# Kernel tuning notes

Measured on AMD Instinct MI355X. Metric: run time of the kernel, lower is better.

The kernel has to match this reference:

```python
import jax, jax.numpy as jnp
import numpy as np

B, C, K, L = 2, 64, 256, 128
H = 8
DH = C // H
PROJ = 64
DADP = 10
FFT = 8
NG = 4
EPS = 1e-5
SCALE = float(1.0 / np.sqrt(DH))


def group_norm(x, g, b):
    # x: (B, C, N); GroupNorm(4, C)
    bb, cc, nn = x.shape
    xg = x.reshape(bb, NG, cc // NG, nn)
    mu = jnp.mean(xg, axis=(2, 3), keepdims=True)
    var = jnp.var(xg, axis=(2, 3), keepdims=True)
    xn = ((xg - mu) * jax.lax.rsqrt(var + EPS)).reshape(bb, cc, nn)
    return xn * g[None, :, None] + b[None, :, None]


def layer_norm(x, g, b):
    mu = jnp.mean(x, axis=-1, keepdims=True)
    var = jnp.var(x, axis=-1, keepdims=True)
    return (x - mu) * jax.lax.rsqrt(var + EPS) * g + b


def setup_inputs() -> dict:
    key = jax.random.key(0)
    ks = jax.random.split(key, 24)
    it = iter(ks)

    def nrm(shape, scale=0.05):
        return jax.random.normal(next(it), shape, dtype=jnp.float32) * scale

    z = lambda *s: jnp.zeros(s, jnp.float32)
    o = lambda *s: jnp.ones(s, jnp.float32)
    inp = dict(
        y=jax.random.normal(next(it), (B, C, K * L), dtype=jnp.float32),
        a1=jax.nn.softmax(jax.random.normal(next(it), (K, K), dtype=jnp.float32), axis=1),
        a2=jax.nn.softmax(jax.random.normal(next(it), (K, K), dtype=jnp.float32), axis=1),
        nodevec1=nrm((K, DADP), 0.3), nodevec2=nrm((DADP, K), 0.3),
        gcn_w=nrm((C, 7 * C)), gcn_b=z(C),
        s_wq=nrm((C, C)), s_wk=nrm((C, C)), s_wv=nrm((C, C)),
        s_pk=nrm((K, PROJ), float(1.0 / np.sqrt(PROJ))),
        s_pv=nrm((K, PROJ), float(1.0 / np.sqrt(PROJ))),
        s_wo=nrm((C, C)), s_bo=z(C),
        t_wq=nrm((C, C)), t_wk=nrm((C, C)), t_wv=nrm((C, C)),
        t_bq=z(C), t_bk=z(C), t_bv=z(C),
        t_wo=nrm((C, C)), t_bo=z(C),
        t_l1w=nrm((C, FFT)), t_l1b=z(FFT), t_l2w=nrm((FFT, C)), t_l2b=z(C),
        t_ln1g=o(C), t_ln1b=z(C), t_ln2g=o(C), t_ln2b=z(C),
        gn_local_g=o(C), gn_local_b=z(C),
        gn_s_g=o(C), gn_s_b=z(C),
        gn_t_g=o(C), gn_t_b=z(C),
        ff1_w=nrm((C, 2 * C)), ff1_b=z(2 * C),
        ff2_w=nrm((2 * C, C)), ff2_b=z(C),
        gn2_g=o(C), gn2_b=z(C),
        base_B=B, base_K=K, base_L=L,
    )
    return inp


def reference(y, a1, a2, nodevec1, nodevec2, gcn_w, gcn_b,
              s_wq, s_wk, s_wv, s_pk, s_pv, s_wo, s_bo,
              t_wq, t_wk, t_wv, t_bq, t_bk, t_bv, t_wo, t_bo,
              t_l1w, t_l1b, t_l2w, t_l2b, t_ln1g, t_ln1b, t_ln2g, t_ln2b,
              gn_local_g, gn_local_b, gn_s_g, gn_s_b, gn_t_g, gn_t_b,
              ff1_w, ff1_b, ff2_w, ff2_b, gn2_g, gn2_b,
              base_B, base_K, base_L):
    Bv, Kv, Lv = int(base_B), int(base_K), int(base_L)
    y4 = y.reshape(Bv, C, Kv, Lv)

    # ---- AdaptiveGCN: order-2 conv over [a1, a2, adaptive adj] + self ----
    x = y4.transpose(0, 3, 1, 2)  # (B, L, C, K)
    adp = jax.nn.softmax(jax.nn.relu(nodevec1 @ nodevec2), axis=1)  # (K, K)
    outs = [x]
    for a in (a1, a2, adp):
        x1 = jnp.einsum('blcv,wv->blcw', x, a)
        x2 = jnp.einsum('blcv,wv->blcw', x1, a)
        outs += [x1, x2]
    cat = jnp.concatenate(outs, axis=2)  # (B, L, 7C, K)
    g = jnp.einsum('blik,oi->blok', cat, gcn_w) + gcn_b[None, None, :, None]
    y_local = g.transpose(0, 2, 3, 1).reshape(Bv, C, Kv * Lv)
    y_local = group_norm(y + y_local, gn_local_g, gn_local_b)

    # ---- Linformer-style spatial attention over K ----
    xs = y4.transpose(0, 3, 2, 1).reshape(Bv * Lv, Kv, C)  # (B*L, K, C)
    q = (xs @ s_wq).reshape(-1, Kv, H, DH).transpose(0, 2, 1, 3)
    kp = jnp.einsum('bnd,nk->bkd', xs @ s_wk, s_pk).reshape(-1, PROJ, H, DH).transpose(0, 2, 1, 3)
    vp = jnp.einsum('bnd,nk->bkd', xs @ s_wv, s_pv).reshape(-1, PROJ, H, DH).transpose(0, 2, 1, 3)
    attn = jax.nn.softmax(jnp.einsum('bhnd,bhkd->bhnk', q, kp) * SCALE, axis=-1)
    o = jnp.einsum('bhnk,bhkd->bhnd', attn, vp).transpose(0, 2, 1, 3).reshape(-1, Kv, C)
    o = o @ s_wo + s_bo
    y_s = o.transpose(0, 2, 1).reshape(Bv, Lv, C, Kv).transpose(0, 2, 3, 1).reshape(Bv, C, Kv * Lv)
    y_s = group_norm(y + y_s, gn_s_g, gn_s_b)

    # ---- temporal transformer encoder layer over L ----
    xt = y4.transpose(0, 2, 3, 1).reshape(Bv * Kv, Lv, C)  # (B*K, L, C)
    tq = (xt @ t_wq + t_bq).reshape(-1, Lv, H, DH).transpose(0, 2, 1, 3)
    tk = (xt @ t_wk + t_bk).reshape(-1, Lv, H, DH).transpose(0, 2, 1, 3)
    tv = (xt @ t_wv + t_bv).reshape(-1, Lv, H, DH).transpose(0, 2, 1, 3)
    ta = jax.nn.softmax(jnp.einsum('bhnd,bhkd->bhnk', tq, tk) * SCALE, axis=-1)
    to = jnp.einsum('bhnk,bhkd->bhnd', ta, tv).transpose(0, 2, 1, 3).reshape(-1, Lv, C)
    to = to @ t_wo + t_bo
    src = layer_norm(xt + to, t_ln1g, t_ln1b)
    ff = jax.nn.gelu(src @ t_l1w + t_l1b, approximate=False) @ t_l2w + t_l2b
    src = layer_norm(src + ff, t_ln2g, t_ln2b)
    y_t = src.transpose(0, 2, 1).reshape(Bv, Kv, C, Lv).transpose(0, 2, 1, 3).reshape(Bv, C, Kv * Lv)
    y_t = group_norm(y + y_t, gn_t_g, gn_t_b)

    # ---- fuse + channel FFN + final norm ----
    y_in2 = y_local + y_s + y_t
    h = jax.nn.relu(y_in2.transpose(0, 2, 1) @ ff1_w + ff1_b)
    h = (h @ ff2_w + ff2_b).transpose(0, 2, 1)
    return group_norm(h + y_in2, gn2_g, gn2_b)
```

## Files before the change

### kernel.cpp

```cpp
#include <hip/hip_runtime.h>
#include <hip/hip_bf16.h>
#include <math.h>

constexpr int CC = 64, KK = 256, LL = 128;
constexpr int NN = KK * LL;
constexpr int PR = 64;
constexpr int CPG = 16;
constexpr float EPSV = 1e-5f;
constexpr float SCL = 0.35355339059327373f;

typedef __attribute__((ext_vector_type(8))) short short8;
typedef __attribute__((ext_vector_type(4))) float f32x4;

__device__ __forceinline__ unsigned short f2bf(float x) {
  __hip_bfloat16 h = __float2bfloat16(x);
  union { __hip_bfloat16 b; unsigned short u; } v; v.b = h;
  return v.u;
}
__device__ __forceinline__ float bf2f(unsigned short x) {
  union { unsigned int u; float f; } v; v.u = ((unsigned int)x) << 16;
  return v.f;
}

__global__ __launch_bounds__(256) void k_adp(const float* __restrict__ nv1,
                                             const float* __restrict__ nv2,
                                             unsigned short* __restrict__ adp_bf) {
  int w = blockIdx.x, v = threadIdx.x;
  float s = 0.f;
  for (int d = 0; d < 10; ++d) s += nv1[w * 10 + d] * nv2[d * KK + v];
  s = fmaxf(s, 0.f);
  __shared__ float red[256];
  red[v] = s; __syncthreads();
  for (int off = 128; off; off >>= 1) { if (v < off) red[v] = fmaxf(red[v], red[v + off]); __syncthreads(); }
  float m = red[0]; __syncthreads();
  float e = expf(s - m);
  red[v] = e; __syncthreads();
  for (int off = 128; off; off >>= 1) { if (v < off) red[v] += red[v + off]; __syncthreads(); }
  adp_bf[w * KK + v] = f2bf(e / red[0]);
}

__global__ __launch_bounds__(256) void k_castW(const float* __restrict__ s0, const float* __restrict__ s1,
                                               const float* __restrict__ s2,
                                               const float* __restrict__ swo, const float* __restrict__ two,
                                               const float* __restrict__ f1, const float* __restrict__ f2,
                                               const float* __restrict__ swq, const float* __restrict__ swk,
                                               const float* __restrict__ swv,
                                               const float* __restrict__ twq, const float* __restrict__ twk,
                                               const float* __restrict__ twv,
                                               const float* __restrict__ pk, const float* __restrict__ pv,
                                               unsigned short* __restrict__ d0, unsigned short* __restrict__ d1,
                                               unsigned short* __restrict__ d2,
                                               unsigned short* __restrict__ swoT, unsigned short* __restrict__ twoT,
                                               unsigned short* __restrict__ ff1T, unsigned short* __restrict__ ff2T,
                                               unsigned short* __restrict__ swqT, unsigned short* __restrict__ swkT,
                                               unsigned short* __restrict__ swvT,
                                               unsigned short* __restrict__ twqT, unsigned short* __restrict__ twkT,
                                               unsigned short* __restrict__ twvT,
                                               unsigned short* __restrict__ PkT, unsigned short* __restrict__ PvT) {
  int i = blockIdx.x * 256 + threadIdx.x;
  if (i < 65536) d0[i] = f2bf(s0[i]);
  else if (i < 131072) d1[i - 65536] = f2bf(s1[i - 65536]);
  else if (i < 159744) d2[i - 131072] = f2bf(s2[i - 131072]);
  else if (i >= 163840) {
    int j = i - 163840;
    if (j < 4096) { int r = j >> 6, c = j & 63; swoT[c * 64 + r] = f2bf(swo[j]); }
    else if (j < 8192) { int q = j - 4096; int r = q >> 6, c = q & 63; twoT[c * 64 + r] = f2bf(two[q]); }
    else if (j < 16384) { int q = j - 8192; int r = q >> 7, c = q & 127; ff1T[c * 64 + r] = f2bf(f1[q]); }
    else if (j < 24576) { int q = j - 16384; int r = q >> 6, c = q & 63; ff2T[c * 128 + r] = f2bf(f2[q]); }
    else if (j < 28672) { int q = j - 24576; int r = q >> 6, c = q & 63; swqT[c * 64 + r] = f2bf(swq[q]); }
    else if (j < 32768) { int q = j - 28672; int r = q >> 6, c = q & 63; swkT[c * 64 + r] = f2bf(swk[q]); }
    else if (j < 36864) { int q = j - 32768; int r = q >> 6, c = q & 63; swvT[c * 64 + r] = f2bf(swv[q]); }
    else if (j < 40960) { int q = j - 36864; int r = q >> 6, c = q & 63; twqT[c * 64 + r] = f2bf(twq[q]); }
    else if (j < 45056) { int q = j - 40960; int r = q >> 6, c = q & 63; twkT[c * 64 + r] = f2bf(twk[q]); }
    else if (j < 49152) { int q = j - 45056; int r = q >> 6, c = q & 63; twvT[c * 64 + r] = f2bf(twv[q]); }
    else if (j < 65536) { int q = j - 49152; int n = q >> 6, c = q & 63; PkT[c * 256 + n] = f2bf(pk[q]); }
    else if (j < 81920) { int q = j - 65536; int n = q >> 6, c = q & 63; PvT[c * 256 + n] = f2bf(pv[q]); }
  }
}

__global__ __launch_bounds__(64) void k_mix0(const unsigned short* __restrict__ Xbf,
                                             const unsigned short* __restrict__ Wbf,
                                             const float* __restrict__ bias,
                                             unsigned short* __restrict__ s0) {
  int pb = blockIdx.x;
  int lh = pb & 1;
  int k = (pb >> 1) & 255;
  int b = pb >> 9;
  int lane = threadIdx.x;
  int lr = lane & 15, g = lane >> 4;
  short8 af[4][2], bfv[4][2];
#pragma unroll
  for (int ot = 0; ot < 4; ++ot)
#pragma unroll
    for (int kc = 0; kc < 2; ++kc)
      af[ot][kc] = *(const short8*)(Wbf + (size_t)(ot * 16 + lr) * 448 + kc * 32 + g * 8);
#pragma unroll
  for (int ct = 0; ct < 4; ++ct)
#pragma unroll
    for (int kc = 0; kc < 2; ++kc)
      bfv[ct][kc] = *(const short8*)(Xbf + ((size_t)(b * 128 + lh * 64 + ct * 16 + lr) * 256 + k) * 64 + kc * 32 + g * 8);
  f32x4 acc[4][4];
#pragma unroll
  for (int ot = 0; ot < 4; ++ot)
#pragma unroll
    for (int ct = 0; ct < 4; ++ct) acc[ot][ct] = f32x4{0.f, 0.f, 0.f, 0.f};
#pragma unroll
  for (int kc = 0; kc < 2; ++kc)
#pragma unroll
    for (int ot = 0; ot < 4; ++ot)
#pragma unroll
      for (int ct = 0; ct < 4; ++ct)
        acc[ot][ct] = __builtin_amdgcn_mfma_f32_16x16x32_bf16(af[ot][kc], bfv[ct][kc], acc[ot][ct], 0, 0, 0);
#pragma unroll
  for (int ot = 0; ot < 4; ++ot)
#pragma unroll
    for (int ct = 0; ct < 4; ++ct) {
#pragma unroll
      for (int reg = 0; reg < 4; ++reg) {
        int o = ot * 16 + g * 4 + reg;
        s0[(size_t)(b * 64 + o) * NN + (size_t)k * 128 + lh * 64 + ct * 16 + lr] = f2bf(acc[ot][ct][reg] + bias[o]);
      }
    }
}

__global__ __launch_bounds__(64) void k_mix6(const unsigned short* __restrict__ Xbf,
                                             const unsigned short* __restrict__ Wbf,
                                             unsigned short* __restrict__ U1, unsigned short* __restrict__ U2,
                                             unsigned short* __restrict__ U3, unsigned short* __restrict__ U4,
                                             unsigned short* __restrict__ U5, unsigned short* __restrict__ U6) {
  int pb = blockIdx.x;
  int sy = blockIdx.y;
  int b = pb >> 9;
  int rem = pb & 511;
  int l = rem >> 2;
  int kq = (rem & 3) * 64;
  size_t posbase = ((size_t)(b * 128 + l)) * 256 + kq;
  int lane = threadIdx.x;
  int lr = lane & 15, g = lane >> 4;

  short8 af[4][2];
#pragma unroll
  for (int rt = 0; rt < 4; ++rt)
#pragma unroll
    for (int kc = 0; kc < 2; ++kc)
      af[rt][kc] = *(const short8*)(Xbf + (posbase + rt * 16 + lr) * 64 + kc * 32 + g * 8);

  for (int si = 0; si < 2; ++si) {
    int s = sy * 2 + 1 + si;
    short8 bfv[4][2];
#pragma unroll
    for (int ct = 0; ct < 4; ++ct)
#pragma unroll
      for (int kc = 0; kc < 2; ++kc)
        bfv[ct][kc] = *(const short8*)(Wbf + (size_t)(ct * 16 + lr) * 448 + s * 64 + kc * 32 + g * 8);
    f32x4 acc[4][4];
#pragma unroll
    for (int rt = 0; rt < 4; ++rt)
#pragma unroll
      for (int ct = 0; ct < 4; ++ct) acc[rt][ct] = f32x4{0.f, 0.f, 0.f, 0.f};
#pragma unroll
    for (int kc = 0; kc < 2; ++kc)
#pragma unroll
      for (int rt = 0; rt < 4; ++rt)
#pragma unroll
        for (int ct = 0; ct < 4; ++ct)
          acc[rt][ct] = __builtin_amdgcn_mfma_f32_16x16x32_bf16(af[rt][kc], bfv[ct][kc], acc[rt][ct], 0, 0, 0);
    unsigned short* dst = (s == 1) ? U1 : (s == 2) ? U2 : (s == 3) ? U3
                        : (s == 4) ? U4 : (s == 5) ? U5 : U6;
#pragma unroll
    for (int rt = 0; rt < 4; ++rt)
#pragma unroll
      for (int ct = 0; ct < 4; ++ct) {
        int o = ct * 16 + lr;
        int k = kq + rt * 16 + g * 4;
        ushort4 pk;
        pk.x = f2bf(acc[rt][ct][0]); pk.y = f2bf(acc[rt][ct][1]);
        pk.z = f2bf(acc[rt][ct][2]); pk.w = f2bf(acc[rt][ct][3]);
        *(ushort4*)&dst[((size_t)(b * 64 + o) * 128 + l) * 256 + k] = pk;
      }
  }
}

__global__ __launch_bounds__(256) void k_adj2M(const unsigned short* __restrict__ Abf,
                                               const unsigned short* __restrict__ Ueven,
                                               const unsigned short* __restrict__ Uodd,
                                               unsigned short* __restrict__ out) {
  __shared__ unsigned short sH[32 * 256];
  int lq = blockIdx.x & 3, bc = blockIdx.x >> 2;
  int tid = threadIdx.x, wid = tid >> 6, lane = tid & 63;
  int lr = lane & 15, g = lane >> 4;
  int wbase = wid * 64;
  const unsigned short* aP = Abf + (size_t)(wbase + lr) * 256 + g * 8;
  const unsigned short* bP = Ueven + ((size_t)bc * 128 + lq * 32 + lr) * 256 + g * 8;

  f32x4 acc[4][2];
#pragma unroll
  for (int i = 0; i < 4; ++i)
#pragma unroll
    for (int j = 0; j < 2; ++j) acc[i][j] = f32x4{0.f, 0.f, 0.f, 0.f};
  for (int k0 = 0; k0 < 256; k0 += 32) {
    short8 af[4], bfv[2];
#pragma unroll
    for (int i = 0; i < 4; ++i) af[i] = *(const short8*)(aP + (size_t)i * 16 * 256 + k0);
#pragma unroll
    for (int i = 0; i < 2; ++i) bfv[i] = *(const short8*)(bP + (size_t)i * 16 * 256 + k0);
#pragma unroll
    for (int rm = 0; rm < 4; ++rm)
#pragma unroll
      for (int cn = 0; cn < 2; ++cn)
        acc[rm][cn] = __builtin_amdgcn_mfma_f32_16x16x32_bf16(af[rm], bfv[cn], acc[rm][cn], 0, 0, 0);
  }
  {
    const unsigned short* aT = Uodd + (size_t)bc * NN + (size_t)(lq * 32) * 256;
#pragma unroll
    for (int rm = 0; rm < 4; ++rm)
#pragma unroll
      for (int cn = 0; cn < 2; ++cn) {
        int l = cn * 16 + lr;
        int v = wbase + rm * 16 + g * 4;
        ushort4 av = *(const ushort4*)&aT[(size_t)l * 256 + v];
        ushort4 pk;
        pk.x = f2bf(acc[rm][cn][0] + bf2f(av.x));
        pk.y = f2bf(acc[rm][cn][1] + bf2f(av.y));
        pk.z = f2bf(acc[rm][cn][2] + bf2f(av.z));
        pk.w = f2bf(acc[rm][cn][3] + bf2f(av.w));
        int bo = ((l * 256 + v) * 2) ^ ((l & 7) << 4);
        *(ushort4*)((char*)sH + bo) = pk;
      }
  }
  __syncthreads();

  f32x4 c2[4][2];
#pragma unroll
  for (int i = 0; i < 4; ++i)
#pragma unroll
    for (int j = 0; j < 2; ++j) c2[i][j] = f32x4{0.f, 0.f, 0.f, 0.f};
  for (int k0 = 0; k0 < 256; k0 += 32) {
    short8 af[4], bfv[2];
#pragma unroll
    for (int i = 0; i < 4; ++i) af[i] = *(const short8*)(aP + (size_t)i * 16 * 256 + k0);
#pragma unroll
    for (int cn = 0; cn < 2; ++cn) {
      int l = cn * 16 + lr;
      int bo = ((l * 256 + k0 + g * 8) * 2) ^ ((l & 7) << 4);
      bfv[cn] = *(const short8*)((char*)sH + bo);
    }
#pragma unroll
    for (int rm = 0; rm < 4; ++rm)
#pragma unroll
      for (int cn = 0; cn < 2; ++cn)
        c2[rm][cn] = __builtin_amdgcn_mfma_f32_16x16x32_bf16(af[rm], bfv[cn], c2[rm][cn], 0, 0, 0);
  }
  unsigned short* dst = out + (size_t)bc * NN + lq * 32;
#pragma unroll
  for (int rm = 0; rm < 4; ++rm)
#pragma unroll
    for (int cn = 0; cn < 2; ++cn) {
      int col = cn * 16 + lr;
      int row = wbase + rm * 16 + g * 4;
#pragma unroll
      for (int j = 0; j < 4; ++j)
        dst[(size_t)(row + j) * 128 + col] = f2bf(c2[rm][cn][j]);
    }
}

__global__ __launch_bounds__(256) void k_tr(const float* __restrict__ src, float* __restrict__ dst,
                                            const float* __restrict__ add,
                                            unsigned short* __restrict__ dstBf,
                                            long sb, long sk, long sc, long sl,
                                            long db, long dk, long dc, long dl, int nC, int nL) {
  int outer = blockIdx.x;
  int b = outer >> 8, k = outer & 255;
  int tilesL = nL >> 5;
  int tC = blockIdx.y / tilesL, tL = blockIdx.y % tilesL;
  int c0 = tC << 5, l0 = tL << 5;
  __shared__ float s[32][33];
  int tx = threadIdx.x & 31, ty = threadIdx.x >> 5;
  const float* sp = src + (long)b * sb + (long)k * sk;
#pragma unroll
  for (int j = 0; j < 4; ++j) {
    int cc = c0 + ty + j * 8;
    s[ty + j * 8][tx] = sp[(long)cc * sc + (long)(l0 + tx) * sl];
  }
  __syncthreads();
  long dbase = (long)b * db + (long)k * dk;
#pragma unroll
  for (int j = 0; j < 4; ++j) {
    int ll = l0 + ty + j * 8;
    long off = dbase + (long)(c0 + tx) * dc + (long)ll * dl;
    float val = s[tx][ty + j * 8];
    if (add) val += add[off];
    if (dst) dst[off] = val;
    if (dstBf) dstBf[off] = f2bf(val);
  }
}

__global__ __launch_bounds__(256) void k_qkvs_M(const unsigned short* __restrict__ Xbf,
                                                const unsigned short* __restrict__ wqT,
                                                const unsigned short* __restrict__ wkT,
                                                const unsigned short* __restrict__ wvT,
                                                unsigned short* __restrict__ qb,
                                                unsigned short* __restrict__ xkT,
                                                unsigned short* __restrict__ xvT) {
  int r0 = blockIdx.x * 64;
  int t = threadIdx.x, w = t >> 6, lane = t & 63;
  int lr = lane & 15, g = lane >> 4;
  const unsigned short* aP = Xbf + (size_t)(r0 + w * 16 + lr) * 64 + g * 8;
  short8 ax0 = *(const short8*)aP;
  short8 ax1 = *(const short8*)(aP + 32);
  {
    f32x4 acc[4];
#pragma unroll
    for (int ct = 0; ct < 4; ++ct) acc[ct] = f32x4{0.f, 0.f, 0.f, 0.f};
#pragma unroll
    for (int ct = 0; ct < 4; ++ct) {
      short8 b0 = *(const short8*)(wqT + (size_t)(ct * 16 + lr) * 64 + g * 8);
      short8 b1 = *(const short8*)(wqT + (size_t)(ct * 16 + lr) * 64 + 32 + g * 8);
      acc[ct] = __builtin_amdgcn_mfma_f32_16x16x32_bf16(ax0, b0, acc[ct], 0, 0, 0);
      acc[ct] = __builtin_amdgcn_mfma_f32_16x16x32_bf16(ax1, b1, acc[ct], 0, 0, 0);
    }
#pragma unroll
    for (int ct = 0; ct < 4; ++ct)
#pragma unroll
      for (int reg = 0; reg < 4; ++reg)
        qb[(size_t)(r0 + w * 16 + g * 4 + reg) * 64 + ct * 16 + lr] = f2bf(acc[ct][reg]);
  }
  short8 bx0[4], bx1[4];
#pragma unroll
  for (int ct = 0; ct < 4; ++ct) {
    const unsigned short* bP = Xbf + (size_t)(r0 + ct * 16 + lr) * 64 + g * 8;
    bx0[ct] = *(const short8*)bP;
    bx1[ct] = *(const short8*)(bP + 32);
  }
  int bl = r0 >> 8, nb = r0 & 255;
#pragma unroll
  for (int which = 0; which < 2; ++which) {
    const unsigned short* WT = which ? wvT : wkT;
    unsigned short* dstb = which ? xvT : xkT;
    short8 aw0 = *(const short8*)(WT + (size_t)(w * 16 + lr) * 64 + g * 8);
    short8 aw1 = *(const short8*)(WT + (size_t)(w * 16 + lr) * 64 + 32 + g * 8);
    f32x4 acc[4];
#pragma unroll
    for (int ct = 0; ct < 4; ++ct) {
      acc[ct] = f32x4{0.f, 0.f, 0.f, 0.f};
      acc[ct] = __builtin_amdgcn_mfma_f32_16x16x32_bf16(aw0, bx0[ct], acc[ct], 0, 0, 0);
      acc[ct] = __builtin_amdgcn_mfma_f32_16x16x32_bf16(aw1, bx1[ct], acc[ct], 0, 0, 0);
    }
#pragma unroll
    for (int ct = 0; ct < 4; ++ct)
#pragma unroll
      for (int reg = 0; reg < 4; ++reg) {
        int o = w * 16 + g * 4 + reg;
        dstb[(size_t)bl * 16384 + (size_t)o * 256 + nb + ct * 16 + lr] = f2bf(acc[ct][reg]);
      }
  }
}

__global__ __launch_bounds__(256) void k_qkvt_M(const unsigned short* __restrict__ Xbf,
                                                const unsigned short* __restrict__ wqT,
                                                const unsigned short* __restrict__ wkT,
                                                const unsigned short* __restrict__ wvT,
                                                const float* __restrict__ bq, const float* __restrict__ bk_,
                                                const float* __restrict__ bv,
                                                unsigned short* __restrict__ qb,
                                                unsigned short* __restrict__ kb,
                                                unsigned short* __restrict__ vt) {
  int r0 = blockIdx.x * 64;
  int t = threadIdx.x, w = t >> 6, lane = t & 63;
  int lr = lane & 15, g = lane >> 4;
  const unsigned short* aP = Xbf + (size_t)(r0 + w * 16 + lr) * 64 + g * 8;
  short8 ax0 = *(const short8*)aP;
  short8 ax1 = *(const short8*)(aP + 32);
#pragma unroll
  for (int which = 0; which < 2; ++which) {
    const unsigned short* WT = which ? wkT : wqT;
    const float* bias = which ? bk_ : bq;
    unsigned short* dstb = which ? kb : qb;
    f32x4 acc[4];
#pragma unroll
    for (int ct = 0; ct < 4; ++ct) {
      acc[ct] = f32x4{0.f, 0.f, 0.f, 0.f};
      short8 b0 = *(const short8*)(WT + (size_t)(ct * 16 + lr) * 64 + g * 8);
      short8 b1 = *(const short8*)(WT + (size_t)(ct * 16 + lr) * 64 + 32 + g * 8);
      acc[ct] = __builtin_amdgcn_mfma_f32_16x16x32_bf16(ax0, b0, acc[ct], 0, 0, 0);
      acc[ct] = __builtin_amdgcn_mfma_f32_16x16x32_bf16(ax1, b1, acc[ct], 0, 0, 0);
    }
#pragma unroll
    for (int ct = 0; ct < 4; ++ct) {
      float bvv = bias[ct * 16 + lr];
#pragma unroll
      for (int reg = 0; reg < 4; ++reg)
        dstb[(size_t)(r0 + w * 16 + g * 4 + reg) * 64 + ct * 16 + lr] = f2bf(acc[ct][reg] + bvv);
    }
  }
  short8 bx0[4], bx1[4];
#pragma unroll
  for (int ct = 0; ct < 4; ++ct) {
    const unsigned short* bP = Xbf + (size_t)(r0 + ct * 16 + lr) * 64 + g * 8;
    bx0[ct] = *(const short8*)bP;
    bx1[ct] = *(const short8*)(bP + 32);
  }
  int bkk = r0 >> 7, lbase = r0 & 127;
  short8 aw0 = *(const short8*)(wvT + (size_t)(w * 16 + lr) * 64 + g * 8);
  short8 aw1 = *(const short8*)(wvT + (size_t)(w * 16 + lr) * 64 + 32 + g * 8);
  f32x4 acc[4];
#pragma unroll
  for (int ct = 0; ct < 4; ++ct) {
    acc[ct] = f32x4{0.f, 0.f, 0.f, 0.f};
    acc[ct] = __builtin_amdgcn_mfma_f32_16x16x32_bf16(aw0, bx0[ct], acc[ct], 0, 0, 0);
    acc[ct] = __builtin_amdgcn_mfma_f32_16x16x32_bf16(aw1, bx1[ct], acc[ct], 0, 0, 0);
  }
  int lb4 = lbase >> 4;
#pragma unroll
  for (int ct = 0; ct < 4; ++ct)
#pragma unroll
    for (int reg = 0; reg < 4; ++reg) {
      int o = w * 16 + g * 4 + reg;
      vt[(size_t)bkk * 8192 + (size_t)o * 128 + lr * 8 + lb4 + ct] = f2bf(acc[ct][reg] + bv[o]);
    }
}

__global__ __launch_bounds__(256) void k_sprojM(const unsigned short* __restrict__ XkT,
                                                const unsigned short* __restrict__ XvT,
                                                const unsigned short* __restrict__ PkT,
                                                const unsigned short* __restrict__ PvT,
                                                unsigned short* __restrict__ kpb,
                                                unsigned short* __restrict__ vptb) {
  int bl = blockIdx.x;
  int which = blockIdx.y;
  int t = threadIdx.x, w = t >> 6, lane = t & 63;
  int lr = lane & 15, g = lane >> 4;
  const unsigned short* Abase = which ? PvT : XkT + (size_t)bl * 16384;
  const unsigned short* Bbase = which ? XvT + (size_t)bl * 16384 : PkT;
  const unsigned short* aP = Abase + (size_t)(w * 16 + lr) * 256 + g * 8;
  f32x4 acc[4];
#pragma unroll
  for (int ct = 0; ct < 4; ++ct) acc[ct] = f32x4{0.f, 0.f, 0.f, 0.f};
  for (int k0 = 0; k0 < 256; k0 += 32) {
    short8 af = *(const short8*)(aP + k0);
#pragma unroll
    for (int ct = 0; ct < 4; ++ct) {
      short8 bf = *(const short8*)(Bbase + (size_t)(ct * 16 + lr) * 256 + k0 + g * 8);
      acc[ct] = __builtin_amdgcn_mfma_f32_16x16x32_bf16(af, bf, acc[ct], 0, 0, 0);
    }
  }
  if (!which) {
    unsigned short* dst = kpb + (size_t)bl * 4096;
#pragma unroll
    for (int ct = 0; ct < 4; ++ct) {
// ... 418 lines not shown
  const float* s_wo  = (const float*)d_in[12];
  const float* s_bo  = (const float*)d_in[13];
  const float* t_wq  = (const float*)d_in[14];
  const float* t_wk  = (const float*)d_in[15];
  const float* t_wv  = (const float*)d_in[16];
  const float* t_bq  = (const float*)d_in[17];
  const float* t_bk  = (const float*)d_in[18];
  const float* t_bv  = (const float*)d_in[19];
  const float* t_wo  = (const float*)d_in[20];
  const float* t_bo  = (const float*)d_in[21];
  const float* t_l1w = (const float*)d_in[22];
  const float* t_l1b = (const float*)d_in[23];
  const float* t_l2w = (const float*)d_in[24];
  const float* t_l2b = (const float*)d_in[25];
  const float* ln1g  = (const float*)d_in[26];
  const float* ln1b  = (const float*)d_in[27];
  const float* ln2g  = (const float*)d_in[28];
  const float* ln2b  = (const float*)d_in[29];
  const float* gnlg  = (const float*)d_in[30];
  const float* gnlb  = (const float*)d_in[31];
  const float* gnsg  = (const float*)d_in[32];
  const float* gnsb  = (const float*)d_in[33];
  const float* gntg  = (const float*)d_in[34];
  const float* gntb  = (const float*)d_in[35];
  const float* ff1w  = (const float*)d_in[36];
  const float* ff1b  = (const float*)d_in[37];
  const float* ff2w  = (const float*)d_in[38];
  const float* ff2b  = (const float*)d_in[39];
  const float* gn2g  = (const float*)d_in[40];
  const float* gn2b  = (const float*)d_in[41];

  float* ws = (float*)d_ws;
  float* part  = ws + 65536;
  unsigned short* a1_bf   = (unsigned short*)(ws + 131072);
  unsigned short* a2_bf   = (unsigned short*)(ws + 163840);
  unsigned short* adp_bf  = (unsigned short*)(ws + 196608);
  unsigned short* gcnw_bf = (unsigned short*)(ws + 229376);
  unsigned short* xs_bf   = (unsigned short*)(ws + 262144);
  unsigned short* swoT = (unsigned short*)(ws + 2359296);
  unsigned short* twoT = (unsigned short*)(ws + 2361344);
  unsigned short* ff1T = (unsigned short*)(ws + 2363392);
  unsigned short* ff2T = (unsigned short*)(ws + 2367488);
  unsigned short* swqT = (unsigned short*)(ws + 2371584);
  unsigned short* swkT = (unsigned short*)(ws + 2373632);
  unsigned short* swvT = (unsigned short*)(ws + 2375680);
  unsigned short* twqT = (unsigned short*)(ws + 2377728);
  unsigned short* twkT = (unsigned short*)(ws + 2379776);
  unsigned short* twvT = (unsigned short*)(ws + 2381824);
  unsigned short* PkT  = (unsigned short*)(ws + 2383872);
  unsigned short* PvT  = (unsigned short*)(ws + 2392064);
  unsigned short* kpb  = (unsigned short*)(ws + 131072);
  unsigned short* vptb = (unsigned short*)(ws + 1179648);
  const size_t SLOT = 4194304;
  float* G0 = ws + SLOT * 1;
  float* G1 = ws + SLOT * 2;
  float* G2 = ws + SLOT * 3;
  float* G3 = ws + SLOT * 4;
  float* G4 = ws + SLOT * 5;
  float* G5 = ws + SLOT * 6;
  float* G6 = ws + SLOT * 7;
  unsigned short* U1 = (unsigned short*)G3;
  unsigned short* U2 = (unsigned short*)G3 + 4194304;
  unsigned short* U3 = (unsigned short*)G4;
  unsigned short* U4 = (unsigned short*)G4 + 4194304;
  unsigned short* U5 = (unsigned short*)G5;
  unsigned short* U6 = (unsigned short*)G5 + 4194304;
  unsigned short* s0bf = (unsigned short*)G1;
  unsigned short* Q1bf = (unsigned short*)G0;
  unsigned short* Q3bf = (unsigned short*)G0 + 4194304;
  unsigned short* Q2bf = (unsigned short*)G6;
  unsigned short* SLb  = (unsigned short*)G3;
  unsigned short* SSb  = (unsigned short*)G1;
  unsigned short* STb  = (unsigned short*)G2;
  unsigned short* qbuf = (unsigned short*)G0;
  unsigned short* xkT = (unsigned short*)G4;
  unsigned short* xvT = (unsigned short*)G5;
  unsigned short* kbuf = (unsigned short*)G4;
  unsigned short* vtbuf = (unsigned short*)G5;
  unsigned short* xt_bf = (unsigned short*)G6;
  float* out = (float*)d_out;

  const long BS = 2097152;

  k_adp<<<256, 256, 0, stream>>>(nv1, nv2, adp_bf);
  k_castW<<<960, 256, 0, stream>>>(a1, a2, gcn_w, s_wo, t_wo, ff1w, ff2w,
                                   s_wq, s_wk, s_wv, t_wq, t_wk, t_wv, s_pk, s_pv,
                                   a1_bf, a2_bf, gcnw_bf, swoT, twoT, ff1T, ff2T,
                                   swqT, swkT, swvT, twqT, twkT, twvT, PkT, PvT);

  k_tr<<<dim3(512, 8), 256, 0, stream>>>(y, nullptr, nullptr, xs_bf, BS, 128, 32768, 1, BS, 64, 1, 16384, 64, 128);

  k_mix0<<<1024, 64, 0, stream>>>(xs_bf, gcnw_bf, gcn_b, s0bf);
  k_mix6<<<dim3(1024, 3), 64, 0, stream>>>(xs_bf, gcnw_bf, U1, U2, U3, U4, U5, U6);
  k_adj2M<<<512, 256, 0, stream>>>(a1_bf, U2, U1, Q1bf);
  k_adj2M<<<512, 256, 0, stream>>>(a2_bf, U4, U3, Q2bf);
  k_adj2M<<<512, 256, 0, stream>>>(adp_bf, U6, U5, Q3bf);
  k_gn_partB<<<dim3(64, 8), 256, 0, stream>>>(y, s0bf, Q1bf, Q2bf, Q3bf, SLb, part);

  k_qkvs_M<<<1024, 256, 0, stream>>>(xs_bf, swqT, swkT, swvT, qbuf, xkT, xvT);
  k_sprojM<<<dim3(256, 2), 256, 0, stream>>>(xkT, xvT, PkT, PvT, kpb, vptb);
  k_attnP<64, 1><<<512, 512, 0, stream>>>(qbuf, kpb, vptb, swoT, s_bo, G4);
  k_tr<<<dim3(512, 8), 256, 0, stream>>>(G4, nullptr, y, SSb, BS, 64, 16384, 1, BS, 128, 1, 32768, 128, 64);
  k_gn_part1B<<<dim3(64, 8), 256, 0, stream>>>(SSb, part + 2048);

  k_tr<<<dim3(512, 8), 256, 0, stream>>>(y, G2, nullptr, xt_bf, BS, 128, 32768, 1, BS, 8192, 1, 64, 64, 128);
  k_qkvt_M<<<1024, 256, 0, stream>>>(xt_bf, twqT, twkT, twvT, t_bq, t_bk, t_bv, qbuf, kbuf, vtbuf);
  k_attnP<128, 0><<<512, 512, 0, stream>>>(qbuf, kbuf, vtbuf, twoT, t_bo, G6);
  k_tffn<<<1024, 256, 0, stream>>>(G2, G6, t_l1w, t_l1b, t_l2w, t_l2b,
                                   ln1g, ln1b, ln2g, ln2b, G0);
  k_tr<<<dim3(512, 8), 256, 0, stream>>>(G0, nullptr, y, STb, BS, 8192, 64, 1, BS, 128, 1, 32768, 128, 64);
  k_gn_part1B<<<dim3(64, 8), 256, 0, stream>>>(STb, part + 4096);

  k_gn_apply3B<<<4096, 256, 0, stream>>>(SLb, SSb, STb, part, gnlg, gnlb, gnsg, gnsb, gntg, gntb, G4);

  k_tr<<<dim3(512, 8), 256, 0, stream>>>(G4, nullptr, nullptr, (unsigned short*)G5,
                                         BS, 128, 32768, 1, BS, 8192, 1, 64, 64, 128);
  k_cffn<<<1024, 256, 0, stream>>>((unsigned short*)G5, ff1T, ff2T, ff1b, ff2b, G6);
  k_tr<<<dim3(512, 8), 256, 0, stream>>>(G6, out, G4, nullptr, BS, 8192, 64, 1, BS, 128, 1, 32768, 128, 64);
  k_gn_part<<<dim3(64, 8), 256, 0, stream>>>(out, part);
  k_gn_apply<<<4096, 256, 0, stream>>>(out, part, gn2g, gn2b, out);
}
```

Measured before the change: 338.7 us.

## Merge independent kernels into combined launches to cut launch count

```diff
diff --git a/kernel.cpp b/kernel.cpp
--- a/kernel.cpp
+++ b/kernel.cpp
@@ -22,24 +22,7 @@
   return v.f;
 }
 
-__global__ __launch_bounds__(256) void k_adp(const float* __restrict__ nv1,
-                                             const float* __restrict__ nv2,
-                                             unsigned short* __restrict__ adp_bf) {
-  int w = blockIdx.x, v = threadIdx.x;
-  float s = 0.f;
-  for (int d = 0; d < 10; ++d) s += nv1[w * 10 + d] * nv2[d * KK + v];
-  s = fmaxf(s, 0.f);
-  __shared__ float red[256];
-  red[v] = s; __syncthreads();
-  for (int off = 128; off; off >>= 1) { if (v < off) red[v] = fmaxf(red[v], red[v + off]); __syncthreads(); }
-  float m = red[0]; __syncthreads();
-  float e = expf(s - m);
-  red[v] = e; __syncthreads();
-  for (int off = 128; off; off >>= 1) { if (v < off) red[v] += red[v + off]; __syncthreads(); }
-  adp_bf[w * KK + v] = f2bf(e / red[0]);
-}
-
-__global__ __launch_bounds__(256) void k_castW(const float* __restrict__ s0, const float* __restrict__ s1,
+__global__ __launch_bounds__(256) void k_setup(const float* __restrict__ s0, const float* __restrict__ s1,
                                                const float* __restrict__ s2,
                                                const float* __restrict__ swo, const float* __restrict__ two,
                                                const float* __restrict__ f1, const float* __restrict__ f2,
@@ -48,6 +31,7 @@
                                                const float* __restrict__ twq, const float* __restrict__ twk,
                                                const float* __restrict__ twv,
                                                const float* __restrict__ pk, const float* __restrict__ pv,
+                                               const float* __restrict__ nv1, const float* __restrict__ nv2,
                                                unsigned short* __restrict__ d0, unsigned short* __restrict__ d1,
                                                unsigned short* __restrict__ d2,
                                                unsigned short* __restrict__ swoT, unsigned short* __restrict__ twoT,
@@ -56,135 +40,159 @@
                                                unsigned short* __restrict__ swvT,
                                                unsigned short* __restrict__ twqT, unsigned short* __restrict__ twkT,
                                                unsigned short* __restrict__ twvT,
-                                               unsigned short* __restrict__ PkT, unsigned short* __restrict__ PvT) {
-  int i = blockIdx.x * 256 + threadIdx.x;
-  if (i < 65536) d0[i] = f2bf(s0[i]);
-  else if (i < 131072) d1[i - 65536] = f2bf(s1[i - 65536]);
-  else if (i < 159744) d2[i - 131072] = f2bf(s2[i - 131072]);
-  else if (i >= 163840) {
-    int j = i - 163840;
-    if (j < 4096) { int r = j >> 6, c = j & 63; swoT[c * 64 + r] = f2bf(swo[j]); }
-    else if (j < 8192) { int q = j - 4096; int r = q >> 6, c = q & 63; twoT[c * 64 + r] = f2bf(two[q]); }
-    else if (j < 16384) { int q = j - 8192; int r = q >> 7, c = q & 127; ff1T[c * 64 + r] = f2bf(f1[q]); }
-    else if (j < 24576) { int q = j - 16384; int r = q >> 6, c = q & 63; ff2T[c * 128 + r] = f2bf(f2[q]); }
-    else if (j < 28672) { int q = j - 24576; int r = q >> 6, c = q & 63; swqT[c * 64 + r] = f2bf(swq[q]); }
-    else if (j < 32768) { int q = j - 28672; int r = q >> 6, c = q & 63; swkT[c * 64 + r] = f2bf(swk[q]); }
-    else if (j < 36864) { int q = j - 32768; int r = q >> 6, c = q & 63; swvT[c * 64 + r] = f2bf(swv[q]); }
-    else if (j < 40960) { int q = j - 36864; int r = q >> 6, c = q & 63; twqT[c * 64 + r] = f2bf(twq[q]); }
-    else if (j < 45056) { int q = j - 40960; int r = q >> 6, c = q & 63; twkT[c * 64 + r] = f2bf(twk[q]); }
-    else if (j < 49152) { int q = j - 45056; int r = q >> 6, c = q & 63; twvT[c * 64 + r] = f2bf(twv[q]); }
-    else if (j < 65536) { int q = j - 49152; int n = q >> 6, c = q & 63; PkT[c * 256 + n] = f2bf(pk[q]); }
-    else if (j < 81920) { int q = j - 65536; int n = q >> 6, c = q & 63; PvT[c * 256 + n] = f2bf(pv[q]); }
-  }
-}
-
-__global__ __launch_bounds__(64) void k_mix0(const unsigned short* __restrict__ Xbf,
-                                             const unsigned short* __restrict__ Wbf,
-                                             const float* __restrict__ bias,
-                                             unsigned short* __restrict__ s0) {
-  int pb = blockIdx.x;
-  int lh = pb & 1;
-  int k = (pb >> 1) & 255;
-  int b = pb >> 9;
+                                               unsigned short* __restrict__ PkT, unsigned short* __restrict__ PvT,
+                                               unsigned short* __restrict__ adp_bf) {
+  __shared__ float red[256];
+  if (blockIdx.x < 960) {
+    int i = blockIdx.x * 256 + threadIdx.x;
+    if (i < 65536) d0[i] = f2bf(s0[i]);
+    else if (i < 131072) d1[i - 65536] = f2bf(s1[i - 65536]);
+    else if (i < 159744) d2[i - 131072] = f2bf(s2[i - 131072]);
+    else if (i >= 163840) {
+      int j = i - 163840;
+      if (j < 4096) { int r = j >> 6, c = j & 63; swoT[c * 64 + r] = f2bf(swo[j]); }
+      else if (j < 8192) { int q = j - 4096; int r = q >> 6, c = q & 63; twoT[c * 64 + r] = f2bf(two[q]); }
+      else if (j < 16384) { int q = j - 8192; int r = q >> 7, c = q & 127; ff1T[c * 64 + r] = f2bf(f1[q]); }
+      else if (j < 24576) { int q = j - 16384; int r = q >> 6, c = q & 63; ff2T[c * 128 + r] = f2bf(f2[q]); }
+      else if (j < 28672) { int q = j - 24576; int r = q >> 6, c = q & 63; swqT[c * 64 + r] = f2bf(swq[q]); }
+      else if (j < 32768) { int q = j - 28672; int r = q >> 6, c = q & 63; swkT[c * 64 + r] = f2bf(swk[q]); }
+      else if (j < 36864) { int q = j - 32768; int r = q >> 6, c = q & 63; swvT[c * 64 + r] = f2bf(swv[q]); }
+      else if (j < 40960) { int q = j - 36864; int r = q >> 6, c = q & 63; twqT[c * 64 + r] = f2bf(twq[q]); }
+      else if (j < 45056) { int q = j - 40960; int r = q >> 6, c = q & 63; twkT[c * 64 + r] = f2bf(twk[q]); }
+      else if (j < 49152) { int q = j - 45056; int r = q >> 6, c = q & 63; twvT[c * 64 + r] = f2bf(twv[q]); }
+      else if (j < 65536) { int q = j - 49152; int n = q >> 6, c = q & 63; PkT[c * 256 + n] = f2bf(pk[q]); }
+      else if (j < 81920) { int q = j - 65536; int n = q >> 6, c = q & 63; PvT[c * 256 + n] = f2bf(pv[q]); }
+    }
+  } else {
+    int w = blockIdx.x - 960, v = threadIdx.x;
+    float s = 0.f;
+    for (int d = 0; d < 10; ++d) s += nv1[w * 10 + d] * nv2[d * KK + v];
+    s = fmaxf(s, 0.f);
+    red[v] = s; __syncthreads();
+    for (int off = 128; off; off >>= 1) { if (v < off) red[v] = fmaxf(red[v], red[v + off]); __syncthreads(); }
+    float m = red[0]; __syncthreads();
+    float e = expf(s - m);
+    red[v] = e; __syncthreads();
+    for (int off = 128; off; off >>= 1) { if (v < off) red[v] += red[v + off]; __syncthreads(); }
+    adp_bf[w * KK + v] = f2bf(e / red[0]);
+  }
+}
+
+__global__ __launch_bounds__(64) void k_mixall(const unsigned short* __restrict__ Xbf,
+                                               const unsigned short* __restrict__ Wbf,
+                                               const float* __restrict__ bias,
+                                               unsigned short* __restrict__ s0out,
+                                               unsigned short* __restrict__ U1, unsigned short* __restrict__ U2,
+                                               unsigned short* __restrict__ U3, unsigned short* __restrict__ U4,
+                                               unsigned short* __restrict__ U5, unsigned short* __restrict__ U6) {
   int lane = threadIdx.x;
   int lr = lane & 15, g = lane >> 4;
-  short8 af[4][2], bfv[4][2];
-#pragma unroll
-  for (int ot = 0; ot < 4; ++ot)
+  if (blockIdx.x < 1024) {
+    int pb = blockIdx.x;
+    int lh = pb & 1;
+    int k = (pb >> 1) & 255;
+    int b = pb >> 9;
+    short8 af[4][2], bfv[4][2];
+#pragma unroll
+    for (int ot = 0; ot < 4; ++ot)
+#pragma unroll
+      for (int kc = 0; kc < 2; ++kc)
+        af[ot][kc] = *(const short8*)(Wbf + (size_t)(ot * 16 + lr) * 448 + kc * 32 + g * 8);
+#pragma unroll
+    for (int ct = 0; ct < 4; ++ct)
+#pragma unroll
+      for (int kc = 0; kc < 2; ++kc)
+        bfv[ct][kc] = *(const short8*)(Xbf + ((size_t)(b * 128 + lh * 64 + ct * 16 + lr) * 256 + k) * 64 + kc * 32 + g * 8);
+    f32x4 acc[4][4];
+#pragma unroll
+    for (int ot = 0; ot < 4; ++ot)
+#pragma unroll
+      for (int ct = 0; ct < 4; ++ct) acc[ot][ct] = f32x4{0.f, 0.f, 0.f, 0.f};
 #pragma unroll
     for (int kc = 0; kc < 2; ++kc)
-      af[ot][kc] = *(const short8*)(Wbf + (size_t)(ot * 16 + lr) * 448 + kc * 32 + g * 8);
-#pragma unroll
-  for (int ct = 0; ct < 4; ++ct)
-#pragma unroll
-    for (int kc = 0; kc < 2; ++kc)
-      bfv[ct][kc] = *(const short8*)(Xbf + ((size_t)(b * 128 + lh * 64 + ct * 16 + lr) * 256 + k) * 64 + kc * 32 + g * 8);
-  f32x4 acc[4][4];
-#pragma unroll
-  for (int ot = 0; ot < 4; ++ot)
-#pragma unroll
-    for (int ct = 0; ct < 4; ++ct) acc[ot][ct] = f32x4{0.f, 0.f, 0.f, 0.f};
-#pragma unroll
-  for (int kc = 0; kc < 2; ++kc)
+#pragma unroll
+      for (int ot = 0; ot < 4; ++ot)
+#pragma unroll
+        for (int ct = 0; ct < 4; ++ct)
+          acc[ot][ct] = __builtin_amdgcn_mfma_f32_16x16x32_bf16(af[ot][kc], bfv[ct][kc], acc[ot][ct], 0, 0, 0);
 #pragma unroll
     for (int ot = 0; ot < 4; ++ot)
 #pragma unroll
+      for (int ct = 0; ct < 4; ++ct) {
+#pragma unroll
+        for (int reg = 0; reg < 4; ++reg) {
+          int o = ot * 16 + g * 4 + reg;
+          s0out[(size_t)(b * 64 + o) * NN + (size_t)k * 128 + lh * 64 + ct * 16 + lr] = f2bf(acc[ot][ct][reg] + bias[o]);
+        }
+      }
+  } else {
+    int idx = blockIdx.x - 1024;
+    int pb = idx & 1023;
+    int sy = idx >> 10;
+    int b = pb >> 9;
+    int rem = pb & 511;
+    int l = rem >> 2;
+    int kq = (rem & 3) * 64;
+    size_t posbase = ((size_t)(b * 128 + l)) * 256 + kq;
+
+    short8 af[4][2];
+#pragma unroll
+    for (int rt = 0; rt < 4; ++rt)
+#pragma unroll
+      for (int kc = 0; kc < 2; ++kc)
+        af[rt][kc] = *(const short8*)(Xbf + (posbase + rt * 16 + lr) * 64 + kc * 32 + g * 8);
+
+    for (int si = 0; si < 2; ++si) {
+      int s = sy * 2 + 1 + si;
+      short8 bfv[4][2];
+#pragma unroll
       for (int ct = 0; ct < 4; ++ct)
-        acc[ot][ct] = __builtin_amdgcn_mfma_f32_16x16x32_bf16(af[ot][kc], bfv[ct][kc], acc[ot][ct], 0, 0, 0);
-#pragma unroll
-  for (int ot = 0; ot < 4; ++ot)
-#pragma unroll
-    for (int ct = 0; ct < 4; ++ct) {
-#pragma unroll
-      for (int reg = 0; reg < 4; ++reg) {
-        int o = ot * 16 + g * 4 + reg;
-        s0[(size_t)(b * 64 + o) * NN + (size_t)k * 128 + lh * 64 + ct * 16 + lr] = f2bf(acc[ot][ct][reg] + bias[o]);
-      }
-    }
-}
-
-__global__ __launch_bounds__(64) void k_mix6(const unsigned short* __restrict__ Xbf,
-                                             const unsigned short* __restrict__ Wbf,
-                                             unsigned short* __restrict__ U1, unsigned short* __restrict__ U2,
-                                             unsigned short* __restrict__ U3, unsigned short* __restrict__ U4,
-                                             unsigned short* __restrict__ U5, unsigned short* __restrict__ U6) {
-  int pb = blockIdx.x;
-  int sy = blockIdx.y;
-  int b = pb >> 9;
-  int rem = pb & 511;
-  int l = rem >> 2;
-  int kq = (rem & 3) * 64;
-  size_t posbase = ((size_t)(b * 128 + l)) * 256 + kq;
-  int lane = threadIdx.x;
-  int lr = lane & 15, g = lane >> 4;
-
-  short8 af[4][2];
-#pragma unroll
-  for (int rt = 0; rt < 4; ++rt)
-#pragma unroll
-    for (int kc = 0; kc < 2; ++kc)
-      af[rt][kc] = *(const short8*)(Xbf + (posbase + rt * 16 + lr) * 64 + kc * 32 + g * 8);
-
-  for (int si = 0; si < 2; ++si) {
-    int s = sy * 2 + 1 + si;
-    short8 bfv[4][2];
-#pragma unroll
-    for (int ct = 0; ct < 4; ++ct)
+#pragma unroll
+        for (int kc = 0; kc < 2; ++kc)
+          bfv[ct][kc] = *(const short8*)(Wbf + (size_t)(ct * 16 + lr) * 448 + s * 64 + kc * 32 + g * 8);
+      f32x4 acc[4][4];
+#pragma unroll
+      for (int rt = 0; rt < 4; ++rt)
+#pragma unroll
+        for (int ct = 0; ct < 4; ++ct) acc[rt][ct] = f32x4{0.f, 0.f, 0.f, 0.f};
 #pragma unroll
       for (int kc = 0; kc < 2; ++kc)
-        bfv[ct][kc] = *(const short8*)(Wbf + (size_t)(ct * 16 + lr) * 448 + s * 64 + kc * 32 + g * 8);
-    f32x4 acc[4][4];
-#pragma unroll
-    for (int rt = 0; rt < 4; ++rt)
-#pragma unroll
-      for (int ct = 0; ct < 4; ++ct) acc[rt][ct] = f32x4{0.f, 0.f, 0.f, 0.f};
-#pragma unroll
-    for (int kc = 0; kc < 2; ++kc)
+#pragma unroll
+        for (int rt = 0; rt < 4; ++rt)
+#pragma unroll
+          for (int ct = 0; ct < 4; ++ct)
+            acc[rt][ct] = __builtin_amdgcn_mfma_f32_16x16x32_bf16(af[rt][kc], bfv[ct][kc], acc[rt][ct], 0, 0, 0);
+      unsigned short* dst = (s == 1) ? U1 : (s == 2) ? U2 : (s == 3) ? U3
+                          : (s == 4) ? U4 : (s == 5) ? U5 : U6;
 #pragma unroll
       for (int rt = 0; rt < 4; ++rt)
 #pragma unroll
-        for (int ct = 0; ct < 4; ++ct)
-          acc[rt][ct] = __builtin_amdgcn_mfma_f32_16x16x32_bf16(af[rt][kc], bfv[ct][kc], acc[rt][ct], 0, 0, 0);
-    unsigned short* dst = (s == 1) ? U1 : (s == 2) ? U2 : (s == 3) ? U3
-                        : (s == 4) ? U4 : (s == 5) ? U5 : U6;
-#pragma unroll
-    for (int rt = 0; rt < 4; ++rt)
-#pragma unroll
-      for (int ct = 0; ct < 4; ++ct) {
-        int o = ct * 16 + lr;
-        int k = kq + rt * 16 + g * 4;
-        ushort4 pk;
-        pk.x = f2bf(acc[rt][ct][0]); pk.y = f2bf(acc[rt][ct][1]);
-        pk.z = f2bf(acc[rt][ct][2]); pk.w = f2bf(acc[rt][ct][3]);
-        *(ushort4*)&dst[((size_t)(b * 64 + o) * 128 + l) * 256 + k] = pk;
-      }
-  }
-}
-
-__global__ __launch_bounds__(256) void k_adj2M(const unsigned short* __restrict__ Abf,
-                                               const unsigned short* __restrict__ Ueven,
-                                               const unsigned short* __restrict__ Uodd,
-                                               unsigned short* __restrict__ out) {
+        for (int ct = 0; ct < 4; ++ct) {
+          int o = ct * 16 + lr;
+          int k = kq + rt * 16 + g * 4;
+          ushort4 pk;
+          pk.x = f2bf(acc[rt][ct][0]); pk.y = f2bf(acc[rt][ct][1]);
+          pk.z = f2bf(acc[rt][ct][2]); pk.w = f2bf(acc[rt][ct][3]);
+          *(ushort4*)&dst[((size_t)(b * 64 + o) * 128 + l) * 256 + k] = pk;
+        }
+    }
+  }
+}
+
+__global__ __launch_bounds__(256) void k_adj3(const unsigned short* __restrict__ A0,
+                                              const unsigned short* __restrict__ A1,
+                                              const unsigned short* __restrict__ A2,
+                                              const unsigned short* __restrict__ U1, const unsigned short* __restrict__ U2,
+                                              const unsigned short* __restrict__ U3, const unsigned short* __restrict__ U4,
+                                              const unsigned short* __restrict__ U5, const unsigned short* __restrict__ U6,
+                                              unsigned short* __restrict__ O0, unsigned short* __restrict__ O1,
+                                              unsigned short* __restrict__ O2) {
+  int which = blockIdx.y;
+  const unsigned short* Abf = (which == 0) ? A0 : (which == 1) ? A1 : A2;
+  const unsigned short* Ueven = (which == 0) ? U2 : (which == 1) ? U4 : U6;
+  const unsigned short* Uodd  = (which == 0) ? U1 : (which == 1) ? U3 : U5;
+  unsigned short* out = (which == 0) ? O0 : (which == 1) ? O1 : O2;
+
   __shared__ unsigned short sH[32 * 256];
   int lq = blockIdx.x & 3, bc = blockIdx.x >> 2;
   int tid = threadIdx.x, wid = tid >> 6, lane = tid & 63;
@@ -295,13 +303,42 @@
   }
 }
 
-__global__ __launch_bounds__(256) void k_qkvs_M(const unsigned short* __restrict__ Xbf,
-                                                const unsigned short* __restrict__ wqT,
-                                                const unsigned short* __restrict__ wkT,
-                                                const unsigned short* __restrict__ wvT,
-                                                unsigned short* __restrict__ qb,
-                                                unsigned short* __restrict__ xkT,
-                                                unsigned short* __restrict__ xvT) {
+__global__ __launch_bounds__(256) void k_qkvs_tr(const unsigned short* __restrict__ Xbf,
+                                                 const unsigned short* __restrict__ wqT,
+                                                 const unsigned short* __restrict__ wkT,
+                                                 const unsigned short* __restrict__ wvT,
+                                                 unsigned short* __restrict__ qb,
+                                                 unsigned short* __restrict__ xkT,
+                                                 unsigned short* __restrict__ xvT,
+                                                 const float* __restrict__ y,
+                                                 float* __restrict__ xtF,
+                                                 unsigned short* __restrict__ xtBf) {
+  __shared__ float sTile[32][33];
+  if (blockIdx.x >= 1024) {
+    int tb = blockIdx.x - 1024;
+    int outer = tb >> 3, yy = tb & 7;
+    int b = outer >> 8, k = outer & 255;
+    int tC = yy >> 2, tL = yy & 3;
+    int c0 = tC << 5, l0 = tL << 5;
+    int tx = threadIdx.x & 31, ty = threadIdx.x >> 5;
+    const float* sp = y + (long)b * 2097152 + (long)k * 128;
+#pragma unroll
+    for (int j = 0; j < 4; ++j) {
+      int cc = c0 + ty + j * 8;
+      sTile[ty + j * 8][tx] = sp[(long)cc * 32768 + (long)(l0 + tx)];
+    }
+    __syncthreads();
+    long dbase = (long)b * 2097152 + (long)k * 8192;
+#pragma unroll
+    for (int j = 0; j < 4; ++j) {
+      int ll = l0 + ty + j * 8;
+      long off = dbase + (long)(c0 + tx) + (long)ll * 64;
+      float val = sTile[tx][ty + j * 8];
+      xtF[off] = val;
+      xtBf[off] = f2bf(val);
+    }
+    return;
+  }
   int r0 = blockIdx.x * 64;
   int t = threadIdx.x, w = t >> 6, lane = t & 63;
   int lr = lane & 15, g = lane >> 4;
@@ -356,15 +393,35 @@
   }
 }
 
-__global__ __launch_bounds__(256) void k_qkvt_M(const unsigned short* __restrict__ Xbf,
-                                                const unsigned short* __restrict__ wqT,
-                                                const unsigned short* __restrict__ wkT,
-                                                const unsigned short* __restrict__ wvT,
-                                                const float* __restrict__ bq, const float* __restrict__ bk_,
-                                                const float* __restrict__ bv,
-                                                unsigned short* __restrict__ qb,
-                                                unsigned short* __restrict__ kb,
-                                                unsigned short* __restrict__ vt) {
+__global__ __launch_bounds__(256) void k_qkvt_gn(const unsigned short* __restrict__ Xbf,
+                                                 const unsigned short* __restrict__ wqT,
+                                                 const unsigned short* __restrict__ wkT,
+                                                 const unsigned short* __restrict__ wvT,
+                                                 const float* __restrict__ bq, const float* __restrict__ bk_,
+                                                 const float* __restrict__ bv,
+                                                 unsigned short* __restrict__ qb,
+                                                 unsigned short* __restrict__ kb,
+                                                 unsigned short* __restrict__ vt,
+                                                 const unsigned short* __restrict__ gnIn,
+                                                 float* __restrict__ gnPart) {
+  __shared__ float rs[256], rq[256];
+  if (blockIdx.x >= 1024) {
+    int tb = blockIdx.x - 1024;
+    int blk = tb & 63, bg = tb >> 6, t = threadIdx.x;
+    size_t start = (size_t)bg * ((size_t)CPG * NN) + (size_t)blk * 8192;
+    const ushort4* q0 = (const ushort4*)(gnIn + start);
+    float s = 0.f, ss = 0.f;
+    for (int i = t; i < 2048; i += 256) {
+      ushort4 u = q0[i];
+      float a = bf2f(u.x), b = bf2f(u.y), c = bf2f(u.z), d = bf2f(u.w);
+      s += a + b + c + d;
+      ss += a * a + b * b + c * c + d * d;
+    }
+    rs[t] = s; rq[t] = ss; __syncthreads();
+    for (int off = 128; off; off >>= 1) { if (t < off) { rs[t] += rs[t + off]; rq[t] += rq[t + off]; } __syncthreads(); }
+    if (t == 0) { gnPart[(bg * 64 + blk) * 2] = rs[0]; gnPart[(bg * 64 + blk) * 2 + 1] = rq[0]; }
+    return;
+  }
   int r0 = blockIdx.x * 64;
   int t = threadIdx.x, w = t >> 6, lane = t & 63;
   int lr = lane & 15, g = lane >> 4;
@@ -949,29 +1006,25 @@
 
   const long BS = 2097152;
 
-  k_adp<<<256, 256, 0, stream>>>(nv1, nv2, adp_bf);
-  k_castW<<<960, 256, 0, stream>>>(a1, a2, gcn_w, s_wo, t_wo, ff1w, ff2w,
-                                   s_wq, s_wk, s_wv, t_wq, t_wk, t_wv, s_pk, s_pv,
-                                   a1_bf, a2_bf, gcnw_bf, swoT, twoT, ff1T, ff2T,
-                                   swqT, swkT, swvT, twqT, twkT, twvT, PkT, PvT);
+  k_setup<<<1216, 256, 0, stream>>>(a1, a2, gcn_w, s_wo, t_wo, ff1w, ff2w,
+                                    s_wq, s_wk, s_wv, t_wq, t_wk, t_wv, s_pk, s_pv, nv1, nv2,
+                                    a1_bf, a2_bf, gcnw_bf, swoT, twoT, ff1T, ff2T,
+                                    swqT, swkT, swvT, twqT, twkT, twvT, PkT, PvT, adp_bf);
 
   k_tr<<<dim3(512, 8), 256, 0, stream>>>(y, nullptr, nullptr, xs_bf, BS, 128, 32768, 1, BS, 64, 1, 16384, 64, 128);
 
-  k_mix0<<<1024, 64, 0, stream>>>(xs_bf, gcnw_bf, gcn_b, s0bf);
-  k_mix6<<<dim3(1024, 3), 64, 0, stream>>>(xs_bf, gcnw_bf, U1, U2, U3, U4, U5, U6);
-  k_adj2M<<<512, 256, 0, stream>>>(a1_bf, U2, U1, Q1bf);
-  k_adj2M<<<512, 256, 0, stream>>>(a2_bf, U4, U3, Q2bf);
-  k_adj2M<<<512, 256, 0, stream>>>(adp_bf, U6, U5, Q3bf);
+  k_mixall<<<4096, 64, 0, stream>>>(xs_bf, gcnw_bf, gcn_b, s0bf, U1, U2, U3, U4, U5, U6);
+  k_adj3<<<dim3(512, 3), 256, 0, stream>>>(a1_bf, a2_bf, adp_bf, U1, U2, U3, U4, U5, U6,
+                                           Q1bf, Q2bf, Q3bf);
   k_gn_partB<<<dim3(64, 8), 256, 0, stream>>>(y, s0bf, Q1bf, Q2bf, Q3bf, SLb, part);
 
-  k_qkvs_M<<<1024, 256, 0, stream>>>(xs_bf, swqT, swkT, swvT, qbuf, xkT, xvT);
+  k_qkvs_tr<<<5120, 256, 0, stream>>>(xs_bf, swqT, swkT, swvT, qbuf, xkT, xvT, y, G2, xt_bf);
   k_sprojM<<<dim3(256, 2), 256, 0, stream>>>(xkT, xvT, PkT, PvT, kpb, vptb);
   k_attnP<64, 1><<<512, 512, 0, stream>>>(qbuf, kpb, vptb, swoT, s_bo, G4);
   k_tr<<<dim3(512, 8), 256, 0, stream>>>(G4, nullptr, y, SSb, BS, 64, 16384, 1, BS, 128, 1, 32768, 128, 64);
-  k_gn_part1B<<<dim3(64, 8), 256, 0, stream>>>(SSb, part + 2048);
-
-  k_tr<<<dim3(512, 8), 256, 0, stream>>>(y, G2, nullptr, xt_bf, BS, 128, 32768, 1, BS, 8192, 1, 64, 64, 128);
-  k_qkvt_M<<<1024, 256, 0, stream>>>(xt_bf, twqT, twkT, twvT, t_bq, t_bk, t_bv, qbuf, kbuf, vtbuf);
+
+  k_qkvt_gn<<<1536, 256, 0, stream>>>(xt_bf, twqT, twkT, twvT, t_bq, t_bk, t_bv,
+                                      qbuf, kbuf, vtbuf, SSb, part + 2048);
   k_attnP<128, 0><<<512, 512, 0, stream>>>(qbuf, kbuf, vtbuf, twoT, t_bo, G6);
   k_tffn<<<1024, 256, 0, stream>>>(G2, G6, t_l1w, t_l1b, t_l2w, t_l2b,
                                    ln1g, ln1b, ln2g, ln2b, G0);
```

Result: faster. 323.0 us (-4.6%).
